# Kernel tuning notes

Hardware: AMD Instinct MI355X
Metric: run time of the kernel (lower is better)

## Reference

```python
import jax, jax.numpy as jnp
import numpy as np

N = 30000      # nodes
E = 480000     # edges (no self loops; GATConv adds them)
IN = 256       # in_features
OUT = 128      # out_features == per-head channels (concat=False)
H = 4          # heads
NEG_SLOPE = 0.2


def setup_inputs() -> dict:
    key = jax.random.key(0)
    k = jax.random.split(key, 6)
    x = jax.random.normal(k[0], (N, IN), dtype=jnp.float32)
    src = jax.random.randint(k[1], (E,), 0, N, dtype=jnp.int32)
    # guarantee no self loops (GATConv would strip them before re-adding)
    off = jax.random.randint(k[2], (E,), 1, N, dtype=jnp.int32)
    dst = (src + off) % N
    edge_index = jnp.stack([src, dst])  # [2, E]
    W = jax.random.normal(k[3], (IN, H * OUT), dtype=jnp.float32) / np.float32(np.sqrt(IN))
    att_src = jax.random.normal(k[4], (H, OUT), dtype=jnp.float32) / np.float32(np.sqrt(OUT))
    att_dst = jax.random.normal(k[5], (H, OUT), dtype=jnp.float32) / np.float32(np.sqrt(OUT))
    bias = jnp.zeros((OUT,), dtype=jnp.float32)
    return {"x": x, "edge_index": edge_index, "W": W,
            "att_src": att_src, "att_dst": att_dst, "bias": bias}


def reference(x, edge_index, W, att_src, att_dst, bias):
    n = x.shape[0]
    # dense projection -> per-head features [N, H, C]
    h = (x @ W).reshape(n, H, OUT)
    a_s = jnp.einsum('nhc,hc->nh', h, att_src)  # [N, H]
    a_d = jnp.einsum('nhc,hc->nh', h, att_dst)  # [N, H]
    # add self loops (GATConv default add_self_loops=True)
    loop = jnp.arange(n, dtype=edge_index.dtype)
    src = jnp.concatenate([edge_index[0], loop])  # [Et]
    dst = jnp.concatenate([edge_index[1], loop])  # [Et]
    # per-edge attention logits + LeakyReLU
    alpha = jax.nn.leaky_relu(a_s[src] + a_d[dst], NEG_SLOPE)  # [Et, H]
    # segment softmax over incoming edges of each dst node
    amax = jax.ops.segment_max(alpha, dst, num_segments=n)      # [N, H]
    ex = jnp.exp(alpha - amax[dst])
    denom = jax.ops.segment_sum(ex, dst, num_segments=n)        # [N, H]
    w = ex / denom[dst]                                          # [Et, H]
    # gather source features, weight, scatter-add to dst
    msg = h[src] * w[:, :, None]                                 # [Et, H, C]
    out = jax.ops.segment_sum(msg, dst, num_segments=n)          # [N, H, C]
    # concat=False -> mean over heads, then bias, then module's tanh
    out = out.mean(axis=1) + bias                                # [N, C]
    return jnp.tanh(out)
```

## Files before the change

### kernel.cpp

```cpp
#include <hip/hip_runtime.h>
#include <math.h>

#define IN_F   256
#define OUT_F  128
#define HEADS  4
#define HD     (HEADS * OUT_F)
#define NEG    0.2f
#define CAP    64

typedef __attribute__((ext_vector_type(8))) short short8;
typedef __attribute__((ext_vector_type(4))) float f32x4;

typedef __attribute__((address_space(1))) const void* gp_t;
typedef __attribute__((address_space(3))) void* lp_t;

static __device__ __forceinline__ ushort f2bf(float f) {
    union { float f; unsigned u; } v; v.f = f;
    unsigned r = (v.u + 0x7FFFu + ((v.u >> 16) & 1u)) >> 16;
    return (ushort)r;
}
static __device__ __forceinline__ float bflo(unsigned u) {
    union { unsigned u; float f; } v; v.u = u << 16; return v.f;
}
static __device__ __forceinline__ float bfhi(unsigned u) {
    union { unsigned u; float f; } v; v.u = u & 0xFFFF0000u; return v.f;
}

__global__ __launch_bounds__(256) void cvt_wt(const float* __restrict__ W,
                                              ushort* __restrict__ WT) {
    int idx = blockIdx.x * blockDim.x + threadIdx.x;
    int n = idx >> 8, k = idx & 255;
    WT[idx] = f2bf(W[k * HD + n]);
}
__global__ __launch_bounds__(256) void calc_va(const float* __restrict__ W,
                                               const float* __restrict__ att_src,
                                               const float* __restrict__ att_dst,
                                               float* __restrict__ va_s,
                                               float* __restrict__ va_d) {
    int idx = blockIdx.x * blockDim.x + threadIdx.x;
    int h = idx >> 8, k = idx & 255;
    const float* wr = W + (size_t)k * HD + h * OUT_F;
    const float* as = att_src + h * OUT_F;
    const float* ad = att_dst + h * OUT_F;
    float ss = 0.f, sd = 0.f;
#pragma unroll 8
    for (int c = 0; c < OUT_F; ++c) {
        float w = wr[c];
        ss = fmaf(w, as[c], ss);
        sd = fmaf(w, ad[c], sd);
    }
    va_s[idx] = ss;
    va_d[idx] = sd;
}

__global__ __launch_bounds__(256) void fused_x(const float* __restrict__ X,
                                               const float* __restrict__ va_s,
                                               const float* __restrict__ va_d,
                                               ushort* __restrict__ Xb,
                                               float* __restrict__ a_s,
                                               float* __restrict__ a_d,
                                               int n_nodes) {
    const int lane = threadIdx.x & 63;
    const int node = blockIdx.x * 4 + (threadIdx.x >> 6);
    if (node >= n_nodes) return;
    float4 v = *(const float4*)(X + (size_t)node * IN_F + lane * 4);
    ushort4 o; o.x = f2bf(v.x); o.y = f2bf(v.y); o.z = f2bf(v.z); o.w = f2bf(v.w);
    *(ushort4*)(Xb + (size_t)node * IN_F + lane * 4) = o;

    float ps[HEADS], pd[HEADS];
#pragma unroll
    for (int hd = 0; hd < HEADS; ++hd) {
        float4 s4 = *(const float4*)(va_s + hd * IN_F + lane * 4);
        float4 d4 = *(const float4*)(va_d + hd * IN_F + lane * 4);
        ps[hd] = v.x * s4.x + v.y * s4.y + v.z * s4.z + v.w * s4.w;
        pd[hd] = v.x * d4.x + v.y * d4.y + v.z * d4.z + v.w * d4.w;
    }
#pragma unroll
    for (int off = 32; off > 0; off >>= 1) {
#pragma unroll
        for (int hd = 0; hd < HEADS; ++hd) {
            ps[hd] += __shfl_xor(ps[hd], off, 64);
            pd[hd] += __shfl_xor(pd[hd], off, 64);
        }
    }
    if (lane == 0) {
        float4 s4 = make_float4(ps[0], ps[1], ps[2], ps[3]);
        float4 d4 = make_float4(pd[0], pd[1], pd[2], pd[3]);
        *(float4*)(a_s + node * 4) = s4;
        *(float4*)(a_d + node * 4) = d4;
    }
}

#define GBM 128
#define GBN 128
#define GBK 32

__global__ __launch_bounds__(256) void gemm_mfma(const ushort* __restrict__ Xb,
                                                 const ushort* __restrict__ WT,
                                                 ushort* __restrict__ Hb,
                                                 int n_nodes) {
    __shared__ ushort As[GBM][GBK];
    __shared__ ushort Bs[GBN][GBK];
    const int tid = threadIdx.x;
    const int m0 = blockIdx.y * GBM;
    const int n0 = blockIdx.x * GBN;
    const int wave = tid >> 6, lane = tid & 63;
    const int wm = (wave & 1) * 64, wn = (wave >> 1) * 64;
    const int l15 = lane & 15, quad = lane >> 4;

    const int rr = lane >> 2;
    const int cg = (lane & 3) ^ ((lane >> 3) & 3);
    const int rA = wave * 16 + rr;
    const ushort* gA0 = Xb + (size_t)(m0 + rA) * IN_F + cg * 8;
    const ushort* gA1 = Xb + (size_t)(m0 + 64 + rA) * IN_F + cg * 8;
    const ushort* gB0 = WT + (size_t)(n0 + rA) * IN_F + cg * 8;
    const ushort* gB1 = WT + (size_t)(n0 + 64 + rA) * IN_F + cg * 8;
    ushort* lA0 = &As[wave * 16][0];
    ushort* lA1 = &As[64 + wave * 16][0];
    ushort* lB0 = &Bs[wave * 16][0];
    ushort* lB1 = &Bs[64 + wave * 16][0];

    f32x4 acc[4][4];
#pragma unroll
    for (int i = 0; i < 4; ++i)
#pragma unroll
        for (int j = 0; j < 4; ++j) acc[i][j] = (f32x4){0.f, 0.f, 0.f, 0.f};

    const int ks = (quad ^ ((l15 >> 1) & 3)) * 8;

    for (int k0 = 0; k0 < IN_F; k0 += GBK) {
        __syncthreads();
        __builtin_amdgcn_global_load_lds((gp_t)(gA0 + k0), (lp_t)lA0, 16, 0, 0);
        __builtin_amdgcn_global_load_lds((gp_t)(gA1 + k0), (lp_t)lA1, 16, 0, 0);
        __builtin_amdgcn_global_load_lds((gp_t)(gB0 + k0), (lp_t)lB0, 16, 0, 0);
        __builtin_amdgcn_global_load_lds((gp_t)(gB1 + k0), (lp_t)lB1, 16, 0, 0);
        __syncthreads();

        short8 af[4], bf_[4];
#pragma unroll
        for (int f = 0; f < 4; ++f) {
            af[f]  = *(const short8*)&As[wm + f * 16 + l15][ks];
            bf_[f] = *(const short8*)&Bs[wn + f * 16 + l15][ks];
        }
#pragma unroll
        for (int fm = 0; fm < 4; ++fm)
#pragma unroll
            for (int fn = 0; fn < 4; ++fn)
                acc[fm][fn] = __builtin_amdgcn_mfma_f32_16x16x32_bf16(
                    af[fm], bf_[fn], acc[fm][fn], 0, 0, 0);
    }

#pragma unroll
    for (int fm = 0; fm < 4; ++fm) {
        int gmb = m0 + wm + fm * 16 + quad * 4;
#pragma unroll
        for (int reg = 0; reg < 4; ++reg) {
            int gm = gmb + reg;
            if (gm < n_nodes) {
#pragma unroll
                for (int fn = 0; fn < 4; ++fn)
                    Hb[(size_t)gm * HD + n0 + wn + fn * 16 + l15] =
                        f2bf(acc[fm][fn][reg]);
            }
        }
    }
}

__global__ __launch_bounds__(256) void build_table(const int* __restrict__ src,
                                                   const int* __restrict__ dst,
                                                   int* __restrict__ cursor,
                                                   int* __restrict__ table,
                                                   int n_edges) {
    int e = blockIdx.x * blockDim.x + threadIdx.x;
    if (e >= n_edges) return;
    int d = dst[e];
    int r = atomicAdd(&cursor[d], 1);
    if (r < CAP) table[(size_t)d * CAP + r] = src[e];
}

__global__ __launch_bounds__(256) void gat_agg(const ushort* __restrict__ Hb,
                                               const float* __restrict__ a_s,
                                               const float* __restrict__ a_d,
                                               const int* __restrict__ cursor,
                                               const int* __restrict__ table,
                                               const float* __restrict__ bias,
                                               float* __restrict__ out,
                                               int n_nodes) {
    const int lane = threadIdx.x & 63;
    const int n = blockIdx.x * 4 + (threadIdx.x >> 6);
    if (n >= n_nodes) return;
    int deg = cursor[n]; if (deg > CAP) deg = CAP;
    const int* row = table + (size_t)n * CAP;
    const unsigned* hbase = (const unsigned*)Hb;

    const float4 ad4 = *(const float4*)(a_d + n * 4);
    const float4 as4 = *(const float4*)(a_s + n * 4);
    const float ad[4] = {ad4.x, ad4.y, ad4.z, ad4.w};
    float aself[4];
    {
        const float asn[4] = {as4.x, as4.y, as4.z, as4.w};
#pragma unroll
        for (int hd = 0; hd < 4; ++hd) {
            float al = asn[hd] + ad[hd];
            aself[hd] = al > 0.f ? al : NEG * al;
        }
    }
    const bool act = lane < deg;
    float al[4];
    {
        int s = act ? row[lane] : 0;
        float4 av = *(const float4*)(a_s + s * 4);
        const float as_[4] = {av.x, av.y, av.z, av.w};
#pragma unroll
        for (int hd = 0; hd < 4; ++hd) {
            float a = as_[hd] + ad[hd];
            a = a > 0.f ? a : NEG * a;
            al[hd] = act ? a : -1e30f;
        }
    }
    float m[4];
#pragma unroll
    for (int hd = 0; hd < 4; ++hd) m[hd] = al[hd];
#pragma unroll
    for (int off = 32; off > 0; off >>= 1)
#pragma unroll
        for (int hd = 0; hd < 4; ++hd)
            m[hd] = fmaxf(m[hd], __shfl_xor(m[hd], off, 64));
#pragma unroll
    for (int hd = 0; hd < 4; ++hd) m[hd] = fmaxf(m[hd], aself[hd]);

    float w[4], den[4], es[4];
#pragma unroll
    for (int hd = 0; hd < 4; ++hd) {
        w[hd] = act ? __expf(al[hd] - m[hd]) : 0.f;
        den[hd] = w[hd];
    }
#pragma unroll
    for (int off = 32; off > 0; off >>= 1)
#pragma unroll
        for (int hd = 0; hd < 4; ++hd)
            den[hd] += __shfl_xor(den[hd], off, 64);
    float rdv[4];
#pragma unroll
    for (int hd = 0; hd < 4; ++hd) {
        es[hd] = __expf(aself[hd] - m[hd]);
        rdv[hd] = 1.f / (den[hd] + es[hd]);
    }

    float acc0[4], acc1[4];
    {
        const unsigned* p = hbase + (size_t)n * 256;
#pragma unroll
        for (int hd = 0; hd < 4; ++hd) {
            unsigned u = p[hd * 64 + lane];
            acc0[hd] = es[hd] * bflo(u);
            acc1[hd] = es[hd] * bfhi(u);
        }
    }
    int e = 0;
    for (; e + 8 <= deg; e += 8) {
        int4 ra = *(const int4*)(row + e);
        int4 rb = *(const int4*)(row + e + 4);
        const unsigned* p[8];
        p[0] = hbase + (size_t)ra.x * 256; p[1] = hbase + (size_t)ra.y * 256;
        p[2] = hbase + (size_t)ra.z * 256; p[3] = hbase + (size_t)ra.w * 256;
        p[4] = hbase + (size_t)rb.x * 256; p[5] = hbase + (size_t)rb.y * 256;
        p[6] = hbase + (size_t)rb.z * 256; p[7] = hbase + (size_t)rb.w * 256;
        unsigned u[8][4];
#pragma unroll
        for (int j = 0; j < 8; ++j)
#pragma unroll
            for (int hd = 0; hd < 4; ++hd)
                u[j][hd] = p[j][hd * 64 + lane];
#pragma unroll
        for (int j = 0; j < 8; ++j) {
#pragma unroll
            for (int hd = 0; hd < 4; ++hd) {
                float wv = __shfl(w[hd], e + j, 64);
                acc0[hd] = fmaf(wv, bflo(u[j][hd]), acc0[hd]);
                acc1[hd] = fmaf(wv, bfhi(u[j][hd]), acc1[hd]);
            }
        }
    }
    for (; e < deg; ++e) {
        int s = row[e];
        const unsigned* p = hbase + (size_t)s * 256;
#pragma unroll
        for (int hd = 0; hd < 4; ++hd) {
            unsigned u = p[hd * 64 + lane];
            float wv = __shfl(w[hd], e, 64);
            acc0[hd] = fmaf(wv, bflo(u), acc0[hd]);
            acc1[hd] = fmaf(wv, bfhi(u), acc1[hd]);
        }
    }
    float o0 = 0.f, o1 = 0.f;
#pragma unroll
    for (int hd = 0; hd < 4; ++hd) {
        o0 = fmaf(acc0[hd], rdv[hd], o0);
        o1 = fmaf(acc1[hd], rdv[hd], o1);
    }
    float2 b = *(const float2*)(bias + 2 * lane);
    o0 = 0.25f * o0 + b.x;
    o1 = 0.25f * o1 + b.y;
    float2 ov = make_float2(tanhf(o0), tanhf(o1));
    *(float2*)(out + (size_t)n * OUT_F + 2 * lane) = ov;
}

extern "C" void kernel_launch(void* const* d_in, const int* in_sizes, int n_in,
                              void* d_out, int out_size, void* d_ws, size_t ws_size,
                              hipStream_t stream) {
    const float* x       = (const float*)d_in[0];
    const int*   ei      = (const int*)d_in[1];
    const float* W       = (const float*)d_in[2];
    const float* att_src = (const float*)d_in[3];
    const float* att_dst = (const float*)d_in[4];
    const float* bias    = (const float*)d_in[5];
    float* out = (float*)d_out;

    const int n_nodes = in_sizes[0] / IN_F;
    const int n_edges = in_sizes[1] / 2;
    const int* src = ei;
    const int* dst = ei + n_edges;

    char* ws = (char*)d_ws;
    size_t off = 0;
    auto alloc = [&](size_t bytes) -> void* {
        void* p = ws + off;
        off = (off + bytes + 255) & ~(size_t)255;
        return p;
    };
    ushort* Xb     = (ushort*)alloc((size_t)n_nodes * IN_F * sizeof(ushort));
    ushort* Hb     = (ushort*)alloc((size_t)n_nodes * HD * sizeof(ushort));
    ushort* WT     = (ushort*)alloc((size_t)HD * IN_F * sizeof(ushort));
    float*  va_s   = (float*)alloc((size_t)HEADS * IN_F * sizeof(float));
    float*  va_d   = (float*)alloc((size_t)HEADS * IN_F * sizeof(float));
    float*  a_s    = (float*)alloc((size_t)n_nodes * HEADS * sizeof(float));
    float*  a_d    = (float*)alloc((size_t)n_nodes * HEADS * sizeof(float));
    int*    cursor = (int*)alloc((size_t)n_nodes * sizeof(int));
    int*    table  = (int*)alloc((size_t)n_nodes * CAP * sizeof(int));
    (void)ws_size; (void)n_in; (void)out_size;

    hipMemsetAsync(cursor, 0, (size_t)n_nodes * sizeof(int), stream);

    cvt_wt<<<(HD * IN_F) / 256, 256, 0, stream>>>(W, WT);
    calc_va<<<(HEADS * IN_F) / 256, 256, 0, stream>>>(W, att_src, att_dst, va_s, va_d);
    fused_x<<<(n_nodes + 3) / 4, 256, 0, stream>>>(x, va_s, va_d, Xb, a_s, a_d, n_nodes);
    build_table<<<(n_edges + 255) / 256, 256, 0, stream>>>(src, dst, cursor, table, n_edges);

    dim3 ggrid(HD / GBN, (n_nodes + GBM - 1) / GBM);
    gemm_mfma<<<ggrid, 256, 0, stream>>>(Xb, WT, Hb, n_nodes);

    gat_agg<<<(n_nodes + 3) / 4, 256, 0, stream>>>(Hb, a_s, a_d, cursor, table,
                                                   bias, out, n_nodes);
}
```

Measured before the change: 230.6 us.

## Use 16-byte gathers per lane with LDS-staged attention weights in aggregation

The aggregation kernel now has each lane load one 16-byte chunk (8 bf16 channels of one head) per neighbor instead of four 4-byte loads, so each wave issues fewer, wider gather instructions. The per-edge softmax weights are staged in shared memory rather than broadcast with a shuffle on every edge and head, which needs a block-wide barrier, so out-of-range waves are clamped to a valid node instead of exiting early. Heads are reduced across lanes with xor shuffles at the end, and only 16 lanes write the output, using float4 stores. A 4-edge remainder loop is also added.

```diff
diff --git a/kernel.cpp b/kernel.cpp
--- a/kernel.cpp
+++ b/kernel.cpp
@@ -178,6 +178,16 @@
     if (r < CAP) table[(size_t)d * CAP + r] = src[e];
 }
 
+#define ACCUM(U, WV)                                                   \
+    acc[0] = fmaf((WV), bflo((U).x), acc[0]);                          \
+    acc[1] = fmaf((WV), bfhi((U).x), acc[1]);                          \
+    acc[2] = fmaf((WV), bflo((U).y), acc[2]);                          \
+    acc[3] = fmaf((WV), bfhi((U).y), acc[3]);                          \
+    acc[4] = fmaf((WV), bflo((U).z), acc[4]);                          \
+    acc[5] = fmaf((WV), bfhi((U).z), acc[5]);                          \
+    acc[6] = fmaf((WV), bflo((U).w), acc[6]);                          \
+    acc[7] = fmaf((WV), bfhi((U).w), acc[7]);
+
 __global__ __launch_bounds__(256) void gat_agg(const ushort* __restrict__ Hb,
                                                const float* __restrict__ a_s,
                                                const float* __restrict__ a_d,
@@ -186,12 +196,14 @@
                                                const float* __restrict__ bias,
                                                float* __restrict__ out,
                                                int n_nodes) {
+    __shared__ float ws[4][4 * 68 + 4];
     const int lane = threadIdx.x & 63;
-    const int n = blockIdx.x * 4 + (threadIdx.x >> 6);
-    if (n >= n_nodes) return;
+    const int wid  = threadIdx.x >> 6;
+    int n = blockIdx.x * 4 + wid;
+    const bool valid = n < n_nodes;
+    if (!valid) n = n_nodes - 1;
     int deg = cursor[n]; if (deg > CAP) deg = CAP;
     const int* row = table + (size_t)n * CAP;
-    const unsigned* hbase = (const unsigned*)Hb;
 
     const float4 ad4 = *(const float4*)(a_d + n * 4);
     const float4 as4 = *(const float4*)(a_s + n * 4);
@@ -201,8 +213,8 @@
         const float asn[4] = {as4.x, as4.y, as4.z, as4.w};
 #pragma unroll
         for (int hd = 0; hd < 4; ++hd) {
-            float al = asn[hd] + ad[hd];
-            aself[hd] = al > 0.f ? al : NEG * al;
+            float al0 = asn[hd] + ad[hd];
+            aself[hd] = al0 > 0.f ? al0 : NEG * al0;
         }
     }
     const bool act = lane < deg;
@@ -229,7 +241,7 @@
 #pragma unroll
     for (int hd = 0; hd < 4; ++hd) m[hd] = fmaxf(m[hd], aself[hd]);
 
-    float w[4], den[4], es[4];
+    float w[4], den[4];
 #pragma unroll
     for (int hd = 0; hd < 4; ++hd) {
         w[hd] = act ? __expf(al[hd] - m[hd]) : 0.f;
@@ -240,70 +252,88 @@
 #pragma unroll
         for (int hd = 0; hd < 4; ++hd)
             den[hd] += __shfl_xor(den[hd], off, 64);
-    float rdv[4];
+
+    float es[4], rdv[4];
 #pragma unroll
     for (int hd = 0; hd < 4; ++hd) {
         es[hd] = __expf(aself[hd] - m[hd]);
         rdv[hd] = 1.f / (den[hd] + es[hd]);
     }
 
-    float acc0[4], acc1[4];
+#pragma unroll
+    for (int hd = 0; hd < 4; ++hd) ws[wid][hd * 68 + lane] = w[hd];
+    __syncthreads();
+
+    const int hsel = lane >> 4;
+    const float rdv_h = hsel == 0 ? rdv[0] : hsel == 1 ? rdv[1]
+                      : hsel == 2 ? rdv[2] : rdv[3];
+    const float es_h  = hsel == 0 ? es[0]  : hsel == 1 ? es[1]
+                      : hsel == 2 ? es[2]  : es[3];
+    const float* wrow = &ws[wid][hsel * 68];
+    const uint4* hb4 = (const uint4*)Hb;
+
+    float acc[8];
     {
-        const unsigned* p = hbase + (size_t)n * 256;
-#pragma unroll
-        for (int hd = 0; hd < 4; ++hd) {
-            unsigned u = p[hd * 64 + lane];
-            acc0[hd] = es[hd] * bflo(u);
-            acc1[hd] = es[hd] * bfhi(u);
-        }
+        uint4 u = hb4[(size_t)n * 64 + lane];
+        acc[0] = es_h * bflo(u.x); acc[1] = es_h * bfhi(u.x);
+        acc[2] = es_h * bflo(u.y); acc[3] = es_h * bfhi(u.y);
+        acc[4] = es_h * bflo(u.z); acc[5] = es_h * bfhi(u.z);
+        acc[6] = es_h * bflo(u.w); acc[7] = es_h * bfhi(u.w);
     }
     int e = 0;
     for (; e + 8 <= deg; e += 8) {
         int4 ra = *(const int4*)(row + e);
         int4 rb = *(const int4*)(row + e + 4);
-        const unsigned* p[8];
-        p[0] = hbase + (size_t)ra.x * 256; p[1] = hbase + (size_t)ra.y * 256;
-        p[2] = hbase + (size_t)ra.z * 256; p[3] = hbase + (size_t)ra.w * 256;
-        p[4] = hbase + (size_t)rb.x * 256; p[5] = hbase + (size_t)rb.y * 256;
-        p[6] = hbase + (size_t)rb.z * 256; p[7] = hbase + (size_t)rb.w * 256;
-        unsigned u[8][4];
-#pragma unroll
-        for (int j = 0; j < 8; ++j)
-#pragma unroll
-            for (int hd = 0; hd < 4; ++hd)
-                u[j][hd] = p[j][hd * 64 + lane];
-#pragma unroll
-        for (int j = 0; j < 8; ++j) {
-#pragma unroll
-            for (int hd = 0; hd < 4; ++hd) {
-                float wv = __shfl(w[hd], e + j, 64);
-                acc0[hd] = fmaf(wv, bflo(u[j][hd]), acc0[hd]);
-                acc1[hd] = fmaf(wv, bfhi(u[j][hd]), acc1[hd]);
-            }
-        }
+        uint4 u0 = hb4[(size_t)ra.x * 64 + lane];
+        uint4 u1 = hb4[(size_t)ra.y * 64 + lane];
+        uint4 u2 = hb4[(size_t)ra.z * 64 + lane];
+        uint4 u3 = hb4[(size_t)ra.w * 64 + lane];
+        uint4 u4 = hb4[(size_t)rb.x * 64 + lane];
+        uint4 u5 = hb4[(size_t)rb.y * 64 + lane];
+        uint4 u6 = hb4[(size_t)rb.z * 64 + lane];
+        uint4 u7 = hb4[(size_t)rb.w * 64 + lane];
+        float4 wa = *(const float4*)(wrow + e);
+        float4 wb = *(const float4*)(wrow + e + 4);
+        ACCUM(u0, wa.x); ACCUM(u1, wa.y); ACCUM(u2, wa.z); ACCUM(u3, wa.w);
+        ACCUM(u4, wb.x); ACCUM(u5, wb.y); ACCUM(u6, wb.z); ACCUM(u7, wb.w);
+    }
+    for (; e + 4 <= deg; e += 4) {
+        int4 ra = *(const int4*)(row + e);
+        uint4 u0 = hb4[(size_t)ra.x * 64 + lane];
+        uint4 u1 = hb4[(size_t)ra.y * 64 + lane];
+        uint4 u2 = hb4[(size_t)ra.z * 64 + lane];
+        uint4 u3 = hb4[(size_t)ra.w * 64 + lane];
+        float4 wa = *(const float4*)(wrow + e);
+        ACCUM(u0, wa.x); ACCUM(u1, wa.y); ACCUM(u2, wa.z); ACCUM(u3, wa.w);
     }
     for (; e < deg; ++e) {
-        int s = row[e];
-        const unsigned* p = hbase + (size_t)s * 256;
-#pragma unroll
-        for (int hd = 0; hd < 4; ++hd) {
-            unsigned u = p[hd * 64 + lane];
-            float wv = __shfl(w[hd], e, 64);
-            acc0[hd] = fmaf(wv, bflo(u), acc0[hd]);
-            acc1[hd] = fmaf(wv, bfhi(u), acc1[hd]);
-        }
-    }
-    float o0 = 0.f, o1 = 0.f;
-#pragma unroll
-    for (int hd = 0; hd < 4; ++hd) {
-        o0 = fmaf(acc0[hd], rdv[hd], o0);
-        o1 = fmaf(acc1[hd], rdv[hd], o1);
-    }
-    float2 b = *(const float2*)(bias + 2 * lane);
-    o0 = 0.25f * o0 + b.x;
-    o1 = 0.25f * o1 + b.y;
-    float2 ov = make_float2(tanhf(o0), tanhf(o1));
-    *(float2*)(out + (size_t)n * OUT_F + 2 * lane) = ov;
+        uint4 u = hb4[(size_t)row[e] * 64 + lane];
+        float wv = wrow[e];
+        ACCUM(u, wv);
+    }
+
+#pragma unroll
+    for (int c = 0; c < 8; ++c) {
+        float v = acc[c] * rdv_h;
+        v += __shfl_xor(v, 16, 64);
+        v += __shfl_xor(v, 32, 64);
+        acc[c] = v;
+    }
+    if (valid && lane < 16) {
+        float4 b0 = *(const float4*)(bias + lane * 8);
+        float4 b1 = *(const float4*)(bias + lane * 8 + 4);
+        float4 o0, o1;
+        o0.x = tanhf(0.25f * acc[0] + b0.x);
+        o0.y = tanhf(0.25f * acc[1] + b0.y);
+        o0.z = tanhf(0.25f * acc[2] + b0.z);
+        o0.w = tanhf(0.25f * acc[3] + b0.w);
+        o1.x = tanhf(0.25f * acc[4] + b1.x);
+        o1.y = tanhf(0.25f * acc[5] + b1.y);
+        o1.z = tanhf(0.25f * acc[6] + b1.z);
+        o1.w = tanhf(0.25f * acc[7] + b1.w);
+        *(float4*)(out + (size_t)n * OUT_F + lane * 8) = o0;
+        *(float4*)(out + (size_t)n * OUT_F + lane * 8 + 4) = o1;
+    }
 }
 
 extern "C" void kernel_launch(void* const* d_in, const int* in_sizes, int n_in,
```

After: 224.1 us. 2.8% less time.

## Aggregate raw input features before projection, then apply a single stacked GEMM

Applied to the files above, without the earlier changes.

Reorders the computation so per-head attention-weighted aggregation runs over the 256-wide bf16 input features instead of the 512-wide projected features. The result is a per-node 1024-wide vector (4 heads x 256), which one GEMM against a rearranged weight matrix maps to the 128 outputs, with bias and tanh fused into its epilogue. The gather traffic per edge is halved and the large Hb intermediate is no longer written. In exchange, the aggregation does four times more FMAs per loaded element, a 1024-wide Zb is written and then read back, and the GEMM grid shrinks to one column of blocks with a longer K loop. calc_va is also rewritten as a wave-level reduction.

```diff
diff --git a/kernel.cpp b/kernel.cpp
--- a/kernel.cpp
+++ b/kernel.cpp
@@ -5,6 +5,7 @@
 #define OUT_F  128
 #define HEADS  4
 #define HD     (HEADS * OUT_F)
+#define K2     1024
 #define NEG    0.2f
 #define CAP    64
 
@@ -26,31 +27,35 @@
     union { unsigned u; float f; } v; v.u = u & 0xFFFF0000u; return v.f;
 }
 
-__global__ __launch_bounds__(256) void cvt_wt(const float* __restrict__ W,
-                                              ushort* __restrict__ WT) {
+__global__ __launch_bounds__(256) void cvt_wt2(const float* __restrict__ W,
+                                               ushort* __restrict__ WT2) {
     int idx = blockIdx.x * blockDim.x + threadIdx.x;
-    int n = idx >> 8, k = idx & 255;
-    WT[idx] = f2bf(W[k * HD + n]);
-}
+    int cout = idx >> 10, kk = idx & 1023;
+    int h = kk >> 8, c = kk & 255;
+    WT2[idx] = f2bf(W[(size_t)c * HD + h * OUT_F + cout]);
+}
+
 __global__ __launch_bounds__(256) void calc_va(const float* __restrict__ W,
                                                const float* __restrict__ att_src,
                                                const float* __restrict__ att_dst,
                                                float* __restrict__ va_s,
                                                float* __restrict__ va_d) {
-    int idx = blockIdx.x * blockDim.x + threadIdx.x;
-    int h = idx >> 8, k = idx & 255;
+    const int lane = threadIdx.x & 63;
+    const int p = blockIdx.x * 4 + (threadIdx.x >> 6);
+    const int h = p >> 8;
+    const int k = p & 255;
     const float* wr = W + (size_t)k * HD + h * OUT_F;
-    const float* as = att_src + h * OUT_F;
-    const float* ad = att_dst + h * OUT_F;
-    float ss = 0.f, sd = 0.f;
-#pragma unroll 8
-    for (int c = 0; c < OUT_F; ++c) {
-        float w = wr[c];
-        ss = fmaf(w, as[c], ss);
-        sd = fmaf(w, ad[c], sd);
-    }
-    va_s[idx] = ss;
-    va_d[idx] = sd;
+    float w0 = wr[lane], w1 = wr[lane + 64];
+    float s0 = att_src[h * OUT_F + lane], s1 = att_src[h * OUT_F + lane + 64];
+    float d0 = att_dst[h * OUT_F + lane], d1 = att_dst[h * OUT_F + lane + 64];
+    float ss = w0 * s0 + w1 * s1;
+    float sd = w0 * d0 + w1 * d1;
+#pragma unroll
+    for (int off = 32; off > 0; off >>= 1) {
+        ss += __shfl_xor(ss, off, 64);
+        sd += __shfl_xor(sd, off, 64);
+    }
+    if (lane == 0) { va_s[p] = ss; va_d[p] = sd; }
 }
 
 __global__ __launch_bounds__(256) void fused_x(const float* __restrict__ X,
@@ -91,81 +96,6 @@
     }
 }
 
-#define GBM 128
-#define GBN 128
-#define GBK 32
-
-__global__ __launch_bounds__(256) void gemm_mfma(const ushort* __restrict__ Xb,
-                                                 const ushort* __restrict__ WT,
-                                                 ushort* __restrict__ Hb,
-                                                 int n_nodes) {
-    __shared__ ushort As[GBM][GBK];
-    __shared__ ushort Bs[GBN][GBK];
-    const int tid = threadIdx.x;
-    const int m0 = blockIdx.y * GBM;
-    const int n0 = blockIdx.x * GBN;
-    const int wave = tid >> 6, lane = tid & 63;
-    const int wm = (wave & 1) * 64, wn = (wave >> 1) * 64;
-    const int l15 = lane & 15, quad = lane >> 4;
-
-    const int rr = lane >> 2;
-    const int cg = (lane & 3) ^ ((lane >> 3) & 3);
-    const int rA = wave * 16 + rr;
-    const ushort* gA0 = Xb + (size_t)(m0 + rA) * IN_F + cg * 8;
-    const ushort* gA1 = Xb + (size_t)(m0 + 64 + rA) * IN_F + cg * 8;
-    const ushort* gB0 = WT + (size_t)(n0 + rA) * IN_F + cg * 8;
-    const ushort* gB1 = WT + (size_t)(n0 + 64 + rA) * IN_F + cg * 8;
-    ushort* lA0 = &As[wave * 16][0];
-    ushort* lA1 = &As[64 + wave * 16][0];
-    ushort* lB0 = &Bs[wave * 16][0];
-    ushort* lB1 = &Bs[64 + wave * 16][0];
-
-    f32x4 acc[4][4];
-#pragma unroll
-    for (int i = 0; i < 4; ++i)
-#pragma unroll
-        for (int j = 0; j < 4; ++j) acc[i][j] = (f32x4){0.f, 0.f, 0.f, 0.f};
-
-    const int ks = (quad ^ ((l15 >> 1) & 3)) * 8;
-
-    for (int k0 = 0; k0 < IN_F; k0 += GBK) {
-        __syncthreads();
-        __builtin_amdgcn_global_load_lds((gp_t)(gA0 + k0), (lp_t)lA0, 16, 0, 0);
-        __builtin_amdgcn_global_load_lds((gp_t)(gA1 + k0), (lp_t)lA1, 16, 0, 0);
-        __builtin_amdgcn_global_load_lds((gp_t)(gB0 + k0), (lp_t)lB0, 16, 0, 0);
-        __builtin_amdgcn_global_load_lds((gp_t)(gB1 + k0), (lp_t)lB1, 16, 0, 0);
-        __syncthreads();
-
-        short8 af[4], bf_[4];
-#pragma unroll
-        for (int f = 0; f < 4; ++f) {
-            af[f]  = *(const short8*)&As[wm + f * 16 + l15][ks];
-            bf_[f] = *(const short8*)&Bs[wn + f * 16 + l15][ks];
-        }
-#pragma unroll
-        for (int fm = 0; fm < 4; ++fm)
-#pragma unroll
-            for (int fn = 0; fn < 4; ++fn)
-                acc[fm][fn] = __builtin_amdgcn_mfma_f32_16x16x32_bf16(
-                    af[fm], bf_[fn], acc[fm][fn], 0, 0, 0);
-    }
-
-#pragma unroll
-    for (int fm = 0; fm < 4; ++fm) {
-        int gmb = m0 + wm + fm * 16 + quad * 4;
-#pragma unroll
-        for (int reg = 0; reg < 4; ++reg) {
-            int gm = gmb + reg;
-            if (gm < n_nodes) {
-#pragma unroll
-                for (int fn = 0; fn < 4; ++fn)
-                    Hb[(size_t)gm * HD + n0 + wn + fn * 16 + l15] =
-                        f2bf(acc[fm][fn][reg]);
-            }
-        }
-    }
-}
-
 __global__ __launch_bounds__(256) void build_table(const int* __restrict__ src,
                                                    const int* __restrict__ dst,
                                                    int* __restrict__ cursor,
@@ -178,20 +108,43 @@
     if (r < CAP) table[(size_t)d * CAP + r] = src[e];
 }
 
-__global__ __launch_bounds__(256) void gat_agg(const ushort* __restrict__ Hb,
+#define ACC8(U, WE)                                                         \
+    {                                                                       \
+        float f0 = bflo((U).x), f1 = bfhi((U).x);                           \
+        float f2 = bflo((U).y), f3 = bfhi((U).y);                           \
+        acc[0][0] = fmaf((WE).x, f0, acc[0][0]);                            \
+        acc[0][1] = fmaf((WE).x, f1, acc[0][1]);                            \
+        acc[0][2] = fmaf((WE).x, f2, acc[0][2]);                            \
+        acc[0][3] = fmaf((WE).x, f3, acc[0][3]);                            \
+        acc[1][0] = fmaf((WE).y, f0, acc[1][0]);                            \
+        acc[1][1] = fmaf((WE).y, f1, acc[1][1]);                            \
+        acc[1][2] = fmaf((WE).y, f2, acc[1][2]);                            \
+        acc[1][3] = fmaf((WE).y, f3, acc[1][3]);                            \
+        acc[2][0] = fmaf((WE).z, f0, acc[2][0]);                            \
+        acc[2][1] = fmaf((WE).z, f1, acc[2][1]);                            \
+        acc[2][2] = fmaf((WE).z, f2, acc[2][2]);                            \
+        acc[2][3] = fmaf((WE).z, f3, acc[2][3]);                            \
+        acc[3][0] = fmaf((WE).w, f0, acc[3][0]);                            \
+        acc[3][1] = fmaf((WE).w, f1, acc[3][1]);                            \
+        acc[3][2] = fmaf((WE).w, f2, acc[3][2]);                            \
+        acc[3][3] = fmaf((WE).w, f3, acc[3][3]);                            \
+    }
+
+__global__ __launch_bounds__(256) void gat_agg(const ushort* __restrict__ Xb,
                                                const float* __restrict__ a_s,
                                                const float* __restrict__ a_d,
                                                const int* __restrict__ cursor,
                                                const int* __restrict__ table,
-                                               const float* __restrict__ bias,
-                                               float* __restrict__ out,
+                                               ushort* __restrict__ Zb,
                                                int n_nodes) {
+    __shared__ float4 wse[4][CAP];
     const int lane = threadIdx.x & 63;
-    const int n = blockIdx.x * 4 + (threadIdx.x >> 6);
-    if (n >= n_nodes) return;
+    const int wid  = threadIdx.x >> 6;
+    int n = blockIdx.x * 4 + wid;
+    const bool valid = n < n_nodes;
+    if (!valid) n = n_nodes - 1;
     int deg = cursor[n]; if (deg > CAP) deg = CAP;
     const int* row = table + (size_t)n * CAP;
-    const unsigned* hbase = (const unsigned*)Hb;
 
     const float4 ad4 = *(const float4*)(a_d + n * 4);
     const float4 as4 = *(const float4*)(a_s + n * 4);
@@ -201,8 +154,8 @@
         const float asn[4] = {as4.x, as4.y, as4.z, as4.w};
 #pragma unroll
         for (int hd = 0; hd < 4; ++hd) {
-            float al = asn[hd] + ad[hd];
-            aself[hd] = al > 0.f ? al : NEG * al;
+            float al0 = asn[hd] + ad[hd];
+            aself[hd] = al0 > 0.f ? al0 : NEG * al0;
         }
     }
     const bool act = lane < deg;
@@ -229,7 +182,7 @@
 #pragma unroll
     for (int hd = 0; hd < 4; ++hd) m[hd] = fmaxf(m[hd], aself[hd]);
 
-    float w[4], den[4], es[4];
+    float w[4], den[4];
 #pragma unroll
     for (int hd = 0; hd < 4; ++hd) {
         w[hd] = act ? __expf(al[hd] - m[hd]) : 0.f;
@@ -240,70 +193,148 @@
 #pragma unroll
         for (int hd = 0; hd < 4; ++hd)
             den[hd] += __shfl_xor(den[hd], off, 64);
-    float rdv[4];
+
+    float es[4], rdv[4];
 #pragma unroll
     for (int hd = 0; hd < 4; ++hd) {
         es[hd] = __expf(aself[hd] - m[hd]);
         rdv[hd] = 1.f / (den[hd] + es[hd]);
     }
 
-    float acc0[4], acc1[4];
+    wse[wid][lane] = make_float4(w[0], w[1], w[2], w[3]);
+    __syncthreads();
+
+    const uint2* xb2 = (const uint2*)Xb;
+    float acc[4][4];
     {
-        const unsigned* p = hbase + (size_t)n * 256;
+        uint2 u = xb2[(size_t)n * 64 + lane];
+        float f0 = bflo(u.x), f1 = bfhi(u.x), f2 = bflo(u.y), f3 = bfhi(u.y);
 #pragma unroll
         for (int hd = 0; hd < 4; ++hd) {
-            unsigned u = p[hd * 64 + lane];
-            acc0[hd] = es[hd] * bflo(u);
-            acc1[hd] = es[hd] * bfhi(u);
+            acc[hd][0] = es[hd] * f0;
+            acc[hd][1] = es[hd] * f1;
+            acc[hd][2] = es[hd] * f2;
+            acc[hd][3] = es[hd] * f3;
         }
     }
     int e = 0;
     for (; e + 8 <= deg; e += 8) {
         int4 ra = *(const int4*)(row + e);
         int4 rb = *(const int4*)(row + e + 4);
-        const unsigned* p[8];
-        p[0] = hbase + (size_t)ra.x * 256; p[1] = hbase + (size_t)ra.y * 256;
-        p[2] = hbase + (size_t)ra.z * 256; p[3] = hbase + (size_t)ra.w * 256;
-        p[4] = hbase + (size_t)rb.x * 256; p[5] = hbase + (size_t)rb.y * 256;
-        p[6] = hbase + (size_t)rb.z * 256; p[7] = hbase + (size_t)rb.w * 256;
-        unsigned u[8][4];
-#pragma unroll
-        for (int j = 0; j < 8; ++j)
-#pragma unroll
-            for (int hd = 0; hd < 4; ++hd)
-                u[j][hd] = p[j][hd * 64 + lane];
-#pragma unroll
-        for (int j = 0; j < 8; ++j) {
-#pragma unroll
-            for (int hd = 0; hd < 4; ++hd) {
-                float wv = __shfl(w[hd], e + j, 64);
-                acc0[hd] = fmaf(wv, bflo(u[j][hd]), acc0[hd]);
-                acc1[hd] = fmaf(wv, bfhi(u[j][hd]), acc1[hd]);
+        uint2 u0 = xb2[(size_t)ra.x * 64 + lane];
+        uint2 u1 = xb2[(size_t)ra.y * 64 + lane];
+        uint2 u2 = xb2[(size_t)ra.z * 64 + lane];
+        uint2 u3 = xb2[(size_t)ra.w * 64 + lane];
+        uint2 u4 = xb2[(size_t)rb.x * 64 + lane];
+        uint2 u5 = xb2[(size_t)rb.y * 64 + lane];
+        uint2 u6 = xb2[(size_t)rb.z * 64 + lane];
+        uint2 u7 = xb2[(size_t)rb.w * 64 + lane];
+        float4 w0 = wse[wid][e + 0]; float4 w1 = wse[wid][e + 1];
+        float4 w2 = wse[wid][e + 2]; float4 w3 = wse[wid][e + 3];
+        float4 w4 = wse[wid][e + 4]; float4 w5 = wse[wid][e + 5];
+        float4 w6 = wse[wid][e + 6]; float4 w7 = wse[wid][e + 7];
+        ACC8(u0, w0); ACC8(u1, w1); ACC8(u2, w2); ACC8(u3, w3);
+        ACC8(u4, w4); ACC8(u5, w5); ACC8(u6, w6); ACC8(u7, w7);
+    }
+    for (; e < deg; ++e) {
+        uint2 u = xb2[(size_t)row[e] * 64 + lane];
+        float4 we = wse[wid][e];
+        ACC8(u, we);
+    }
+
+    if (valid) {
+        ushort* zr = Zb + (size_t)n * K2;
+#pragma unroll
+        for (int hd = 0; hd < 4; ++hd) {
+            ushort4 z;
+            z.x = f2bf(acc[hd][0] * rdv[hd]);
+            z.y = f2bf(acc[hd][1] * rdv[hd]);
+            z.z = f2bf(acc[hd][2] * rdv[hd]);
+            z.w = f2bf(acc[hd][3] * rdv[hd]);
+            *(ushort4*)(zr + hd * 256 + lane * 4) = z;
+        }
+    }
+}
+
+#define GBM 128
+#define GBN 128
+#define GBK 32
+
+__global__ __launch_bounds__(256) void gemm2(const ushort* __restrict__ Zb,
+                                             const ushort* __restrict__ WT2,
+                                             const float* __restrict__ bias,
+                                             float* __restrict__ out,
+                                             int n_nodes) {
+    __shared__ ushort As[GBM][GBK];
+    __shared__ ushort Bs[GBN][GBK];
+    const int tid = threadIdx.x;
+    const int m0 = blockIdx.y * GBM;
+    const int n0 = blockIdx.x * GBN;
+    const int wave = tid >> 6, lane = tid & 63;
+    const int wm = (wave & 1) * 64, wn = (wave >> 1) * 64;
+    const int l15 = lane & 15, quad = lane >> 4;
+
+    const int rr = lane >> 2;
+    const int cg = (lane & 3) ^ ((lane >> 3) & 3);
+    const int rA = wave * 16 + rr;
+    const ushort* gA0 = Zb + (size_t)(m0 + rA) * K2 + cg * 8;
+    const ushort* gA1 = Zb + (size_t)(m0 + 64 + rA) * K2 + cg * 8;
+    const ushort* gB0 = WT2 + (size_t)(n0 + rA) * K2 + cg * 8;
+    const ushort* gB1 = WT2 + (size_t)(n0 + 64 + rA) * K2 + cg * 8;
+    ushort* lA0 = &As[wave * 16][0];
+    ushort* lA1 = &As[64 + wave * 16][0];
+    ushort* lB0 = &Bs[wave * 16][0];
+    ushort* lB1 = &Bs[64 + wave * 16][0];
+
+    f32x4 acc[4][4];
+#pragma unroll
+    for (int i = 0; i < 4; ++i)
+#pragma unroll
+        for (int j = 0; j < 4; ++j) acc[i][j] = (f32x4){0.f, 0.f, 0.f, 0.f};
+
+    const int ks = (quad ^ ((l15 >> 1) & 3)) * 8;
+
+    for (int k0 = 0; k0 < K2; k0 += GBK) {
+        __syncthreads();
+        __builtin_amdgcn_global_load_lds((gp_t)(gA0 + k0), (lp_t)lA0, 16, 0, 0);
+        __builtin_amdgcn_global_load_lds((gp_t)(gA1 + k0), (lp_t)lA1, 16, 0, 0);
+        __builtin_amdgcn_global_load_lds((gp_t)(gB0 + k0), (lp_t)lB0, 16, 0, 0);
+        __builtin_amdgcn_global_load_lds((gp_t)(gB1 + k0), (lp_t)lB1, 16, 0, 0);
+        __syncthreads();
+
+        short8 af[4], bf_[4];
+#pragma unroll
+        for (int f = 0; f < 4; ++f) {
+            af[f]  = *(const short8*)&As[wm + f * 16 + l15][ks];
+            bf_[f] = *(const short8*)&Bs[wn + f * 16 + l15][ks];
+        }
+#pragma unroll
+        for (int fm = 0; fm < 4; ++fm)
+#pragma unroll
+            for (int fn = 0; fn < 4; ++fn)
+                acc[fm][fn] = __builtin_amdgcn_mfma_f32_16x16x32_bf16(
+                    af[fm], bf_[fn], acc[fm][fn], 0, 0, 0);
+    }
+
+    float bcol[4];
+#pragma unroll
+    for (int fn = 0; fn < 4; ++fn) bcol[fn] = bias[wn + fn * 16 + l15];
+
+#pragma unroll
+    for (int fm = 0; fm < 4; ++fm) {
+        int gmb = m0 + wm + fm * 16 + quad * 4;
+#pragma unroll
+        for (int reg = 0; reg < 4; ++reg) {
+            int gm = gmb + reg;
+            if (gm < n_nodes) {
+#pragma unroll
+                for (int fn = 0; fn < 4; ++fn) {
+                    float o = tanhf(0.25f * acc[fm][fn][reg] + bcol[fn]);
+                    out[(size_t)gm * OUT_F + wn + fn * 16 + l15] = o;
+                }
             }
         }
     }
-    for (; e < deg; ++e) {
-        int s = row[e];
-        const unsigned* p = hbase + (size_t)s * 256;
-#pragma unroll
-        for (int hd = 0; hd < 4; ++hd) {
-            unsigned u = p[hd * 64 + lane];
-            float wv = __shfl(w[hd], e, 64);
-            acc0[hd] = fmaf(wv, bflo(u), acc0[hd]);
-            acc1[hd] = fmaf(wv, bfhi(u), acc1[hd]);
-        }
-    }
-    float o0 = 0.f, o1 = 0.f;
-#pragma unroll
-    for (int hd = 0; hd < 4; ++hd) {
-        o0 = fmaf(acc0[hd], rdv[hd], o0);
-        o1 = fmaf(acc1[hd], rdv[hd], o1);
-    }
-    float2 b = *(const float2*)(bias + 2 * lane);
-    o0 = 0.25f * o0 + b.x;
-    o1 = 0.25f * o1 + b.y;
-    float2 ov = make_float2(tanhf(o0), tanhf(o1));
-    *(float2*)(out + (size_t)n * OUT_F + 2 * lane) = ov;
 }
 
 extern "C" void kernel_launch(void* const* d_in, const int* in_sizes, int n_in,
@@ -330,8 +361,8 @@
         return p;
     };
     ushort* Xb     = (ushort*)alloc((size_t)n_nodes * IN_F * sizeof(ushort));
-    ushort* Hb     = (ushort*)alloc((size_t)n_nodes * HD * sizeof(ushort));
-    ushort* WT     = (ushort*)alloc((size_t)HD * IN_F * sizeof(ushort));
+    ushort* Zb     = (ushort*)alloc((size_t)n_nodes * K2 * sizeof(ushort));
+    ushort* WT2    = (ushort*)alloc((size_t)OUT_F * K2 * sizeof(ushort));
     float*  va_s   = (float*)alloc((size_t)HEADS * IN_F * sizeof(float));
     float*  va_d   = (float*)alloc((size_t)HEADS * IN_F * sizeof(float));
     float*  a_s    = (float*)alloc((size_t)n_nodes * HEADS * sizeof(float));
@@ -342,14 +373,14 @@
 
     hipMemsetAsync(cursor, 0, (size_t)n_nodes * sizeof(int), stream);
 
-    cvt_wt<<<(HD * IN_F) / 256, 256, 0, stream>>>(W, WT);
-    calc_va<<<(HEADS * IN_F) / 256, 256, 0, stream>>>(W, att_src, att_dst, va_s, va_d);
+    cvt_wt2<<<(OUT_F * K2) / 256, 256, 0, stream>>>(W, WT2);
+    calc_va<<<(HEADS * IN_F) / 4, 256, 0, stream>>>(W, att_src, att_dst, va_s, va_d);
     fused_x<<<(n_nodes + 3) / 4, 256, 0, stream>>>(x, va_s, va_d, Xb, a_s, a_d, n_nodes);
     build_table<<<(n_edges + 255) / 256, 256, 0, stream>>>(src, dst, cursor, table, n_edges);
 
-    dim3 ggrid(HD / GBN, (n_nodes + GBM - 1) / GBM);
-    gemm_mfma<<<ggrid, 256, 0, stream>>>(Xb, WT, Hb, n_nodes);
-
-    gat_agg<<<(n_nodes + 3) / 4, 256, 0, stream>>>(Hb, a_s, a_d, cursor, table,
-                                                   bias, out, n_nodes);
-}
+    gat_agg<<<(n_nodes + 3) / 4, 256, 0, stream>>>(Xb, a_s, a_d, cursor, table,
+                                                   Zb, n_nodes);
+
+    dim3 ggrid(1, (n_nodes + GBM - 1) / GBM);
+    gemm2<<<ggrid, 256, 0, stream>>>(Zb, WT2, bias, out, n_nodes);
+}
```

Result: faster. 216.9 us (-5.9%).
